# Kernel tuning notes

Hardware: AMD Instinct MI355X
Metric: run time of the kernel (lower is better)

Reference implementation:

```python
import jax, jax.numpy as jnp
import numpy as np

N, H, HEADS = 4096, 256, 3
ALPHA = 0.2
NEG_INF = -9e15


def _sign_adj(key, n, density):
    # sparse signed adjacency with +1 on the diagonal (values in {-1,0,1})
    k1, k2 = jax.random.split(key)
    mask = jax.random.uniform(k1, (n, n)) < density
    sign = jnp.where(jax.random.uniform(k2, (n, n)) < 0.5, -1.0, 1.0)
    adj = jnp.where(mask, sign, 0.0).astype(jnp.float32)
    idx = jnp.arange(n)
    return adj.at[idx, idx].set(1.0)


def setup_inputs() -> dict:
    key = jax.random.key(0)
    ks = jax.random.split(key, 16)
    std = 0.01
    gain = 1.414
    return {
        "h": jax.random.normal(ks[0], (N, H), jnp.float32),
        "node_adj": _sign_adj(ks[1], N, 0.005),
        "edge_adj": _sign_adj(ks[2], N, 0.005),
        "gat_W": jax.random.normal(ks[3], (HEADS, H, H), jnp.float32) * (gain / np.sqrt(H, dtype=np.float32)),
        "gat_a": jax.random.normal(ks[4], (HEADS, 2 * H, 1), jnp.float32) * 0.1,
        "edge_Wih": jax.random.normal(ks[5], (3 * H, H), jnp.float32) * std,
        "edge_Whh": jax.random.normal(ks[6], (3 * H, H), jnp.float32) * std,
        "edge_bih": jnp.zeros((3 * H,), jnp.float32),
        "edge_bhh": jnp.zeros((3 * H,), jnp.float32),
        "node_Wih": jax.random.normal(ks[7], (3 * H, H), jnp.float32) * std,
        "node_Whh": jax.random.normal(ks[8], (3 * H, H), jnp.float32) * std,
        "node_bih": jnp.zeros((3 * H,), jnp.float32),
        "node_bhh": jnp.zeros((3 * H,), jnp.float32),
    }


def _gru_cell(x, hstate, Wih, Whh, bih, bhh):
    # torch.nn.GRUCell math, gate order [r, z, n]
    gi = x @ Wih.T + bih
    gh = hstate @ Whh.T + bhh
    ir, iz, inn = jnp.split(gi, 3, axis=1)
    hr, hz, hn = jnp.split(gh, 3, axis=1)
    r = jax.nn.sigmoid(ir + hr)
    z = jax.nn.sigmoid(iz + hz)
    n = jnp.tanh(inn + r * hn)
    return (1.0 - z) * n + z * hstate


def _gat_head(h, node_adj, edge_adj, W, a):
    hW = h @ W  # [N,H]
    hp = (node_adj > 0).astype(hW.dtype) @ hW
    hm = (node_adj < 0).astype(hW.dtype) @ hW
    e_plus = jax.nn.leaky_relu(jnp.concatenate([hp, hm], axis=1) @ a, ALPHA)[:, 0]   # [N]
    e_minus = jax.nn.leaky_relu(jnp.concatenate([hm, hp], axis=1) @ a, ALPHA)[:, 0]  # [N]
    # attention[i, j] depends only on column j (original builds this via repeat)
    att = jnp.where(edge_adj > 0, e_plus[None, :], NEG_INF)
    att = jnp.where(edge_adj < 0, e_minus[None, :], att)
    att = jax.nn.softmax(att, axis=1)
    return (att * edge_adj) @ hW  # concat=False -> no elu


def reference(h, node_adj, edge_adj, gat_W, gat_a,
              edge_Wih, edge_Whh, edge_bih, edge_bhh,
              node_Wih, node_Whh, node_bih, node_bhh):
    dn = jnp.diag(node_adj)  # [N]
    de = jnp.diag(edge_adj)  # [N]
    idx = jnp.arange(node_adj.shape[0])
    node_adj_norm = node_adj.at[idx, idx].add(-dn)  # zero diagonal
    edge_adj_norm = edge_adj.at[idx, idx].add(-de)

    # msg_type == 'diff'
    node_support = node_adj_norm @ h
    edge_output = _gru_cell(node_support, h, edge_Wih, edge_Whh, edge_bih, edge_bhh)

    edge_support = _gat_head(h, node_adj_norm, edge_adj_norm, gat_W[0], gat_a[0])
    for i in range(1, HEADS):
        edge_support = edge_support + _gat_head(h, node_adj_norm, edge_adj_norm, gat_W[i], gat_a[i])
    edge_support = edge_support / HEADS

    node_output = _gru_cell(edge_support, h, node_Wih, node_Whh, node_bih, node_bhh)

    # sp.mm(I_edge, edge_output) + sp.mm(I_node, node_output)
    return de[:, None] * edge_output + dn[:, None] * node_output
```

## Files before the change

kernel.cpp:

```cpp
#include <hip/hip_runtime.h>
#include <hip/hip_bf16.h>
#include <math.h>

#define NN 4096
#define HH 256
#define G3 768
#define NHEADS 3
#define MAXE 128
#define ALPHA 0.2f

typedef __bf16 bf16;
typedef __attribute__((ext_vector_type(2))) __bf16 bf16x2;
typedef __attribute__((ext_vector_type(4))) __bf16 bf16x4;
typedef __attribute__((ext_vector_type(8))) __bf16 bf16x8;
typedef __attribute__((ext_vector_type(4))) float f32x4;

__device__ __forceinline__ void async_copy16(void* lds, const void* g) {
    __builtin_amdgcn_global_load_lds((const __attribute__((address_space(1))) void*)g,
                                     (__attribute__((address_space(3))) void*)lds, 16, 0, 0);
}

__device__ inline float lrelu(float x) { return x > 0.f ? x : ALPHA * x; }
__device__ inline float sigm(float x) { return 1.f / (1.f + __expf(-x)); }

__global__ __launch_bounds__(256) void prep_k(
    const float* __restrict__ h,
    const float* __restrict__ eWih, const float* __restrict__ eWhh,
    const float* __restrict__ nWih, const float* __restrict__ nWhh,
    const float* __restrict__ gat_W, const float* __restrict__ gat_a,
    bf16* __restrict__ hb,
    bf16* __restrict__ Weib, bf16* __restrict__ Wehb,
    bf16* __restrict__ Wnib, bf16* __restrict__ Wnhb,
    bf16* __restrict__ Wtb, float* __restrict__ c0, float* __restrict__ c1) {
    __shared__ float tile[32][33];
    __shared__ float a_s[512];
    int b = blockIdx.x, t = threadIdx.x;
    if (b < 1024) {
        int idx = b * 256 + t;
        float4 v = *(const float4*)(h + (size_t)idx * 4);
        bf16x4 o = {(bf16)v.x, (bf16)v.y, (bf16)v.z, (bf16)v.w};
        *(bf16x4*)(hb + (size_t)idx * 4) = o;
    } else if (b < 1792) {
        int w = (b - 1024) / 192;
        int idx = ((b - 1024) % 192) * 256 + t;
        const float* in = w == 0 ? eWih : (w == 1 ? eWhh : (w == 2 ? nWih : nWhh));
        bf16* outp = w == 0 ? Weib : (w == 1 ? Wehb : (w == 2 ? Wnib : Wnhb));
        float4 v = *(const float4*)(in + (size_t)idx * 4);
        bf16x4 o = {(bf16)v.x, (bf16)v.y, (bf16)v.z, (bf16)v.w};
        *(bf16x4*)(outp + (size_t)idx * 4) = o;
    } else if (b < 1984) {
        int b2 = b - 1792;
        int hd = b2 >> 6, tl = b2 & 63;
        int k0 = (tl >> 3) * 32, n0 = (tl & 7) * 32;
        int tx = t % 32, ty = t / 32;
        const float* Wh = gat_W + (size_t)hd * HH * HH;
        for (int r = ty; r < 32; r += 8) tile[r][tx] = Wh[(size_t)(k0 + r) * HH + n0 + tx];
        __syncthreads();
        bf16* Wth = Wtb + (size_t)hd * HH * HH;
        for (int r = ty; r < 32; r += 8) Wth[(size_t)(n0 + r) * HH + k0 + tx] = (bf16)tile[tx][r];
    } else {
        int hd = b - 1984;
        a_s[t] = gat_a[(size_t)hd * 512 + t];
        a_s[t + 256] = gat_a[(size_t)hd * 512 + 256 + t];
        __syncthreads();
        const float* Wr = gat_W + (size_t)hd * HH * HH + (size_t)t * HH;
        float s0 = 0.f, s1 = 0.f;
        for (int c = 0; c < HH; c++) {
            float w = Wr[c];
            s0 += w * a_s[c];
            s1 += w * a_s[256 + c];
        }
        c0[hd * HH + t] = s0;
        c1[hd * HH + t] = s1;
    }
}

__global__ __launch_bounds__(256) void scan_k(
    const float* __restrict__ node_adj, const float* __restrict__ edge_adj,
    const bf16* __restrict__ hb,
    const float* __restrict__ c0, const float* __restrict__ c1,
    bf16* __restrict__ nsupb, float* __restrict__ dn, float* __restrict__ de,
    float* __restrict__ ep, float* __restrict__ em,
    int* __restrict__ csr_cols, int* __restrict__ csr_nnz) {
    int i = blockIdx.x, t = threadIdx.x;
    int lane = t & 63, wid = t >> 6;
    __shared__ int cnt;
    __shared__ int cols[256];
    __shared__ float part[6][4];
    if (t == 0) cnt = 0;
    __syncthreads();
    bool node = (blockIdx.y == 0);
    const float* row = (node ? node_adj : edge_adj) + (size_t)i * NN;

    float4 v0 = *(const float4*)(row + t * 4);
    float4 v1 = *(const float4*)(row + t * 4 + 1024);
    float4 v2 = *(const float4*)(row + t * 4 + 2048);
    float4 v3 = *(const float4*)(row + t * 4 + 3072);

#define PELEM(A, J) { float a_ = (A); if (a_ != 0.0f) { \
        if ((J) == i) { (node ? dn : de)[i] = a_; } \
        else { int s_ = atomicAdd(&cnt, 1); if (s_ < 256) cols[s_] = (a_ > 0.0f) ? ((J) + 1) : -((J) + 1); } } }
#define PROC(V, OFS) { if ((V).x != 0.f || (V).y != 0.f || (V).z != 0.f || (V).w != 0.f) { \
        int jb_ = t * 4 + (OFS); \
        PELEM((V).x, jb_) PELEM((V).y, jb_ + 1) PELEM((V).z, jb_ + 2) PELEM((V).w, jb_ + 3) } }
    PROC(v0, 0)
    PROC(v1, 1024)
    PROC(v2, 2048)
    PROC(v3, 3072)
#undef PROC
#undef PELEM

    __syncthreads();
    if (node) {
        int n = cnt < 256 ? cnt : 256;
        float accp = 0.f, accm = 0.f;
#pragma unroll 4
        for (int k = 0; k < n; k++) {
            int c = cols[k];
            int j = (c > 0 ? c : -c) - 1;
            float hv = (float)hb[(size_t)j * HH + t];
            if (c > 0) accp += hv; else accm += hv;
        }
        nsupb[(size_t)i * HH + t] = (bf16)(accp - accm);
        float u[6];
#pragma unroll
        for (int hd = 0; hd < NHEADS; hd++) {
            float a0 = c0[hd * HH + t], a1 = c1[hd * HH + t];
            u[hd * 2]     = accp * a0 + accm * a1;
            u[hd * 2 + 1] = accm * a0 + accp * a1;
        }
#pragma unroll
        for (int vv = 0; vv < 6; vv++)
#pragma unroll
            for (int off = 32; off; off >>= 1) u[vv] += __shfl_xor(u[vv], off);
        if (lane == 0)
#pragma unroll
            for (int vv = 0; vv < 6; vv++) part[vv][wid] = u[vv];
        __syncthreads();
        if (t < 6) {
            float s = part[t][0] + part[t][1] + part[t][2] + part[t][3];
            int hd = t >> 1;
            ((t & 1) == 0 ? ep : em)[(size_t)hd * NN + i] = lrelu(s);
        }
    } else {
        int n = cnt < MAXE ? cnt : MAXE;
        if (t == 0) csr_nnz[i] = n;
        for (int k = t; k < n; k += 256) csr_cols[(size_t)i * MAXE + k] = cols[k];
    }
}

__global__ __launch_bounds__(256) void gemm_bt(
    const bf16* __restrict__ A0, const bf16* __restrict__ A1, const bf16* __restrict__ A2,
    const bf16* __restrict__ B0, const bf16* __restrict__ B1, const bf16* __restrict__ B2,
    bf16* __restrict__ C0, bf16* __restrict__ C1, bf16* __restrict__ C2) {
    __shared__ bf16 a_s[128 * 32];
    __shared__ bf16 b_s[128 * 32];
    int z = blockIdx.z;
    const bf16* A = z == 0 ? A0 : (z == 1 ? A1 : A2);
    const bf16* Bt = z == 0 ? B0 : (z == 1 ? B1 : B2);
    bf16* C = z == 0 ? C0 : (z == 1 ? C1 : C2);

    int tid = threadIdx.x;
    int lane = tid & 63, wid = tid >> 6;
    int wr = (wid >> 1) * 64, wc = (wid & 1) * 64;
    int i0 = blockIdx.x * 128;
    int c0n = blockIdx.y * 128;

    f32x4 acc[4][4] = {};
    int kq = (lane >> 4) * 8;

    for (int k0 = 0; k0 < 256; k0 += 32) {
        __syncthreads();
#pragma unroll
        for (int it = 0; it < 2; it++) {
            int ch = it * 256 + tid;
            int r = ch >> 2, c16 = ch & 3;
            async_copy16(&a_s[ch * 8], A + (size_t)(i0 + r) * 256 + k0 + c16 * 8);
            async_copy16(&b_s[ch * 8], Bt + (size_t)(c0n + r) * 256 + k0 + c16 * 8);
        }
        __syncthreads();
        bf16x8 af[4], bf[4];
#pragma unroll
        for (int m = 0; m < 4; m++) af[m] = *(const bf16x8*)&a_s[(wr + m * 16 + (lane & 15)) * 32 + kq];
#pragma unroll
        for (int n = 0; n < 4; n++) bf[n] = *(const bf16x8*)&b_s[(wc + n * 16 + (lane & 15)) * 32 + kq];
#pragma unroll
        for (int m = 0; m < 4; m++)
#pragma unroll
            for (int n = 0; n < 4; n++)
                acc[m][n] = __builtin_amdgcn_mfma_f32_16x16x32_bf16(af[m], bf[n], acc[m][n], 0, 0, 0);
    }
#pragma unroll
    for (int m = 0; m < 4; m++) {
#pragma unroll
        for (int n = 0; n < 4; n++) {
            int row = i0 + wr + m * 16 + (lane >> 4) * 4;
            int col = c0n + wc + n * 16 + (lane & 15);
#pragma unroll
            for (int j = 0; j < 4; j++)
                C[(size_t)(row + j) * G3 + col] = (bf16)acc[m][n][j];
        }
    }
}

__global__ __launch_bounds__(256) void gat_out(
    const int* __restrict__ csr_cols, const int* __restrict__ csr_nnz,
    const float* __restrict__ ep, const float* __restrict__ em,
    const bf16* __restrict__ hWb2, bf16* __restrict__ esupb) {
    int i = blockIdx.x, t = threadIdx.x;
    __shared__ int cols_s[MAXE];
    __shared__ int js[MAXE];
    __shared__ float w_s[NHEADS][MAXE];
    int n = csr_nnz[i];
    if (t < MAXE && t < n) {
        int c = csr_cols[(size_t)i * MAXE + t];
        cols_s[t] = c;
        js[t] = (c > 0 ? c : -c) - 1;
    }
    __syncthreads();
    int wid = t >> 6, lane = t & 63;
    if (wid < NHEADS) {
        int hd = wid;
        const float* eph = ep + (size_t)hd * NN;
        const float* emh = em + (size_t)hd * NN;
        float v0 = -1e30f, v1 = -1e30f;
        if (lane < n)      { int c = cols_s[lane];      v0 = c > 0 ? eph[js[lane]]      : emh[js[lane]]; }
        if (lane + 64 < n) { int c = cols_s[lane + 64]; v1 = c > 0 ? eph[js[lane + 64]] : emh[js[lane + 64]]; }
        float mx = fmaxf(v0, v1);
#pragma unroll
        for (int off = 32; off; off >>= 1) mx = fmaxf(mx, __shfl_xor(mx, off));
        float w0 = (lane < n) ? __expf(v0 - mx) : 0.f;
        float w1 = (lane + 64 < n) ? __expf(v1 - mx) : 0.f;
        float s = w0 + w1;
#pragma unroll
        for (int off = 32; off; off >>= 1) s += __shfl_xor(s, off);
        float inv = 1.f / s;
        if (lane < n)      w_s[hd][lane]      = (cols_s[lane] > 0 ? w0 : -w0) * inv;
        if (lane + 64 < n) w_s[hd][lane + 64] = (cols_s[lane + 64] > 0 ? w1 : -w1) * inv;
    }
    __syncthreads();
    float acc = 0.f;
#pragma unroll
    for (int hd = 0; hd < NHEADS; hd++) {
        const bf16* base = hWb2 + (size_t)hd * HH + t;
#pragma unroll 4
        for (int k = 0; k < n; k++)
            acc += w_s[hd][k] * (float)base[(size_t)js[k] * G3];
    }
    esupb[(size_t)i * HH + t] = (bf16)(acc * (1.f / 3.f));
}

__global__ __launch_bounds__(256) void gru_both(
    const bf16* __restrict__ gie, const bf16* __restrict__ ghe,
    const bf16* __restrict__ gin, const bf16* __restrict__ ghn,
    const float* __restrict__ ebih, const float* __restrict__ ebhh,
    const float* __restrict__ nbih, const float* __restrict__ nbhh,
    const float* __restrict__ h, const float* __restrict__ dnv, const float* __restrict__ dev,
    float* __restrict__ out) {
    int sub = threadIdx.x >> 7, tc = threadIdx.x & 127;
    int i = blockIdx.x * 2 + sub;
    int c = tc * 2;
    size_t gb = (size_t)i * G3;
    float2 hv = *(const float2*)(h + (size_t)i * HH + c);
    float De = dev[i], Dn = dnv[i];

#define LD2(p, off) (*(const bf16x2*)((p) + gb + (off) + c))
#define BI2(p, off) (*(const float2*)((p) + (off) + c))
    bf16x2 eir = LD2(gie, 0), eiz = LD2(gie, 256), ein = LD2(gie, 512);
    bf16x2 ehr = LD2(ghe, 0), ehz = LD2(ghe, 256), ehn = LD2(ghe, 512);
    bf16x2 nir = LD2(gin, 0), niz = LD2(gin, 256), nin = LD2(gin, 512);
    bf16x2 nhr = LD2(ghn, 0), nhz = LD2(ghn, 256), nhn = LD2(ghn, 512);
    float2 ebr = BI2(ebih, 0), ebz = BI2(ebih, 256), ebn = BI2(ebih, 512);
    float2 eb2r = BI2(ebhh, 0), eb2z = BI2(ebhh, 256), eb2n = BI2(ebhh, 512);
    float2 nbr = BI2(nbih, 0), nbz = BI2(nbih, 256), nbn = BI2(nbih, 512);
    float2 nb2r = BI2(nbhh, 0), nb2z = BI2(nbhh, 256), nb2n = BI2(nbhh, 512);
#undef LD2
#undef BI2

    float res[2];
#pragma unroll
    for (int j = 0; j < 2; j++) {
        float hj = j == 0 ? hv.x : hv.y;
        float r = sigm(((float)eir[j] + (j ? ebr.y : ebr.x)) + ((float)ehr[j] + (j ? eb2r.y : eb2r.x)));
        float z = sigm(((float)eiz[j] + (j ? ebz.y : ebz.x)) + ((float)ehz[j] + (j ? eb2z.y : eb2z.x)));
        float nv = tanhf(((float)ein[j] + (j ? ebn.y : ebn.x)) + r * ((float)ehn[j] + (j ? eb2n.y : eb2n.x)));
        float eo = (1.f - z) * nv + z * hj;
        float r2 = sigm(((float)nir[j] + (j ? nbr.y : nbr.x)) + ((float)nhr[j] + (j ? nb2r.y : nb2r.x)));
        float z2 = sigm(((float)niz[j] + (j ? nbz.y : nbz.x)) + ((float)nhz[j] + (j ? nb2z.y : nb2z.x)));
        float nv2 = tanhf(((float)nin[j] + (j ? nbn.y : nbn.x)) + r2 * ((float)nhn[j] + (j ? nb2n.y : nb2n.x)));
        float no = (1.f - z2) * nv2 + z2 * hj;
        res[j] = De * eo + Dn * no;
    }
    *(float2*)(out + (size_t)i * HH + c) = make_float2(res[0], res[1]);
}

extern "C" void kernel_launch(void* const* d_in, const int* in_sizes, int n_in,
                              void* d_out, int out_size, void* d_ws, size_t ws_size,
                              hipStream_t stream) {
    const float* h        = (const float*)d_in[0];
    const float* node_adj = (const float*)d_in[1];
    const float* edge_adj = (const float*)d_in[2];
    const float* gat_W    = (const float*)d_in[3];
    const float* gat_a    = (const float*)d_in[4];
    const float* e_Wih    = (const float*)d_in[5];
    const float* e_Whh    = (const float*)d_in[6];
    const float* e_bih    = (const float*)d_in[7];
    const float* e_bhh    = (const float*)d_in[8];
    const float* n_Wih    = (const float*)d_in[9];
    const float* n_Whh    = (const float*)d_in[10];
    const float* n_bih    = (const float*)d_in[11];
    const float* n_bhh    = (const float*)d_in[12];
    float* out = (float*)d_out;

    char* ws = (char*)d_ws;
    size_t off = 0;
    auto alloc = [&](size_t bytes) { char* p = ws + off; off += (bytes + 255) & ~(size_t)255; return p; };

    float* ep    = (float*)alloc((size_t)NHEADS * NN * 4);
    float* em    = (float*)alloc((size_t)NHEADS * NN * 4);
    float* c0    = (float*)alloc((size_t)NHEADS * HH * 4);
    float* c1    = (float*)alloc((size_t)NHEADS * HH * 4);
    float* dn    = (float*)alloc(NN * 4);
    float* de    = (float*)alloc(NN * 4);
    bf16*  hb    = (bf16*)alloc((size_t)NN * HH * 2);
    bf16*  nsupb = (bf16*)alloc((size_t)NN * HH * 2);
    bf16*  esupb = (bf16*)alloc((size_t)NN * HH * 2);
    bf16*  hWb2  = (bf16*)alloc((size_t)NN * G3 * 2);
    bf16*  gie   = (bf16*)alloc((size_t)NN * G3 * 2);
    bf16*  ghe   = (bf16*)alloc((size_t)NN * G3 * 2);
    bf16*  gin   = (bf16*)alloc((size_t)NN * G3 * 2);
    bf16*  ghn   = (bf16*)alloc((size_t)NN * G3 * 2);
    bf16*  Weib  = (bf16*)alloc((size_t)G3 * HH * 2);
    bf16*  Wehb  = (bf16*)alloc((size_t)G3 * HH * 2);
    bf16*  Wnib  = (bf16*)alloc((size_t)G3 * HH * 2);
    bf16*  Wnhb  = (bf16*)alloc((size_t)G3 * HH * 2);
    bf16*  Wtb   = (bf16*)alloc((size_t)NHEADS * HH * HH * 2);
    int*   csr_cols = (int*)alloc((size_t)NN * MAXE * 4);
    int*   csr_nnz  = (int*)alloc(NN * 4);

    dim3 b256(256);

    prep_k<<<1987, b256, 0, stream>>>(h, e_Wih, e_Whh, n_Wih, n_Whh, gat_W, gat_a,
                                      hb, Weib, Wehb, Wnib, Wnhb, Wtb, c0, c1);

    scan_k<<<dim3(NN, 2), b256, 0, stream>>>(node_adj, edge_adj, hb, c0, c1,
                                             nsupb, dn, de, ep, em, csr_cols, csr_nnz);

    gemm_bt<<<dim3(NN / 128, G3 / 128, 3), b256, 0, stream>>>(
        hb, nsupb, hb, Wtb, Weib, Wehb, hWb2, gie, ghe);

    gat_out<<<NN, b256, 0, stream>>>(csr_cols, csr_nnz, ep, em, hWb2, esupb);

    gemm_bt<<<dim3(NN / 128, G3 / 128, 2), b256, 0, stream>>>(
        esupb, hb, hb, Wnib, Wnhb, Wnhb, gin, ghn, ghn);

    gru_both<<<NN / 2, b256, 0, stream>>>(gie, ghe, gin, ghn,
                                          e_bih, e_bhh, n_bih, n_bhh,
                                          h, dn, de, out);
}
```

Measured before the change: 95.99 us.

## Map one wavefront per adjacency row in scan and vectorize gather loops

```diff
diff --git a/kernel.cpp b/kernel.cpp
--- a/kernel.cpp
+++ b/kernel.cpp
@@ -64,14 +64,17 @@
         a_s[t + 256] = gat_a[(size_t)hd * 512 + 256 + t];
         __syncthreads();
         const float* Wr = gat_W + (size_t)hd * HH * HH + (size_t)t * HH;
-        float s0 = 0.f, s1 = 0.f;
-        for (int c = 0; c < HH; c++) {
-            float w = Wr[c];
-            s0 += w * a_s[c];
-            s1 += w * a_s[256 + c];
-        }
-        c0[hd * HH + t] = s0;
-        c1[hd * HH + t] = s1;
+        f32x4 s0v = {}, s1v = {};
+#pragma unroll 8
+        for (int c4 = 0; c4 < 64; c4++) {
+            f32x4 w = *(const f32x4*)(Wr + c4 * 4);
+            f32x4 a0 = *(const f32x4*)(a_s + c4 * 4);
+            f32x4 a1 = *(const f32x4*)(a_s + 256 + c4 * 4);
+            s0v += w * a0;
+            s1v += w * a1;
+        }
+        c0[hd * HH + t] = s0v[0] + s0v[1] + s0v[2] + s0v[3];
+        c1[hd * HH + t] = s1v[0] + s1v[1] + s1v[2] + s1v[3];
     }
 }
 
@@ -82,70 +85,89 @@
     bf16* __restrict__ nsupb, float* __restrict__ dn, float* __restrict__ de,
     float* __restrict__ ep, float* __restrict__ em,
     int* __restrict__ csr_cols, int* __restrict__ csr_nnz) {
-    int i = blockIdx.x, t = threadIdx.x;
-    int lane = t & 63, wid = t >> 6;
-    __shared__ int cnt;
-    __shared__ int cols[256];
-    __shared__ float part[6][4];
-    if (t == 0) cnt = 0;
-    __syncthreads();
+    int t = threadIdx.x, lane = t & 63, wid = t >> 6;
+    int i = blockIdx.x * 4 + wid;
     bool node = (blockIdx.y == 0);
-    const float* row = (node ? node_adj : edge_adj) + (size_t)i * NN;
-
-    float4 v0 = *(const float4*)(row + t * 4);
-    float4 v1 = *(const float4*)(row + t * 4 + 1024);
-    float4 v2 = *(const float4*)(row + t * 4 + 2048);
-    float4 v3 = *(const float4*)(row + t * 4 + 3072);
-
-#define PELEM(A, J) { float a_ = (A); if (a_ != 0.0f) { \
-        if ((J) == i) { (node ? dn : de)[i] = a_; } \
-        else { int s_ = atomicAdd(&cnt, 1); if (s_ < 256) cols[s_] = (a_ > 0.0f) ? ((J) + 1) : -((J) + 1); } } }
-#define PROC(V, OFS) { if ((V).x != 0.f || (V).y != 0.f || (V).z != 0.f || (V).w != 0.f) { \
-        int jb_ = t * 4 + (OFS); \
-        PELEM((V).x, jb_) PELEM((V).y, jb_ + 1) PELEM((V).z, jb_ + 2) PELEM((V).w, jb_ + 3) } }
-    PROC(v0, 0)
-    PROC(v1, 1024)
-    PROC(v2, 2048)
-    PROC(v3, 3072)
-#undef PROC
-#undef PELEM
-
-    __syncthreads();
+    __shared__ int cnt[4];
+    __shared__ int cols[4][MAXE];
+    if (lane == 0) cnt[wid] = 0;
+    __syncthreads();
+
+    float* dia = node ? dn : de;
+    const float* rp = (node ? node_adj : edge_adj) + (size_t)i * NN + lane * 4;
+
+    f32x4 v0  = *(const f32x4*)(rp);
+    f32x4 v1  = *(const f32x4*)(rp + 256);
+    f32x4 v2  = *(const f32x4*)(rp + 512);
+    f32x4 v3  = *(const f32x4*)(rp + 768);
+    f32x4 v4  = *(const f32x4*)(rp + 1024);
+    f32x4 v5  = *(const f32x4*)(rp + 1280);
+    f32x4 v6  = *(const f32x4*)(rp + 1536);
+    f32x4 v7  = *(const f32x4*)(rp + 1792);
+    f32x4 v8  = *(const f32x4*)(rp + 2048);
+    f32x4 v9  = *(const f32x4*)(rp + 2304);
+    f32x4 v10 = *(const f32x4*)(rp + 2560);
+    f32x4 v11 = *(const f32x4*)(rp + 2816);
+    f32x4 v12 = *(const f32x4*)(rp + 3072);
+    f32x4 v13 = *(const f32x4*)(rp + 3328);
+    f32x4 v14 = *(const f32x4*)(rp + 3584);
+    f32x4 v15 = *(const f32x4*)(rp + 3840);
+
+#define PEL(A, J) { float a_ = (A); if (a_ != 0.0f) { \
+        if ((J) == i) { dia[i] = a_; } \
+        else { int s_ = atomicAdd(&cnt[wid], 1); if (s_ < MAXE) cols[wid][s_] = (a_ > 0.0f) ? ((J) + 1) : -((J) + 1); } } }
+#define PV(V, Q) { if ((V)[0] != 0.f || (V)[1] != 0.f || (V)[2] != 0.f || (V)[3] != 0.f) { \
+        int jb_ = (Q) * 256 + lane * 4; \
+        PEL((V)[0], jb_) PEL((V)[1], jb_ + 1) PEL((V)[2], jb_ + 2) PEL((V)[3], jb_ + 3) } }
+    PV(v0, 0)  PV(v1, 1)  PV(v2, 2)  PV(v3, 3)
+    PV(v4, 4)  PV(v5, 5)  PV(v6, 6)  PV(v7, 7)
+    PV(v8, 8)  PV(v9, 9)  PV(v10, 10) PV(v11, 11)
+    PV(v12, 12) PV(v13, 13) PV(v14, 14) PV(v15, 15)
+#undef PV
+#undef PEL
+
+    __syncthreads();
+    int n = cnt[wid];
+    if (n > MAXE) n = MAXE;
+
     if (node) {
-        int n = cnt < 256 ? cnt : 256;
-        float accp = 0.f, accm = 0.f;
+        f32x4 accp = {}, accm = {};
 #pragma unroll 4
         for (int k = 0; k < n; k++) {
-            int c = cols[k];
+            int c = cols[wid][k];
             int j = (c > 0 ? c : -c) - 1;
-            float hv = (float)hb[(size_t)j * HH + t];
-            if (c > 0) accp += hv; else accm += hv;
-        }
-        nsupb[(size_t)i * HH + t] = (bf16)(accp - accm);
+            bf16x4 hv = *(const bf16x4*)(hb + (size_t)j * HH + lane * 4);
+            f32x4 f = {(float)hv[0], (float)hv[1], (float)hv[2], (float)hv[3]};
+            if (c > 0) accp += f; else accm += f;
+        }
+        f32x4 d = accp - accm;
+        bf16x4 o = {(bf16)d[0], (bf16)d[1], (bf16)d[2], (bf16)d[3]};
+        *(bf16x4*)(nsupb + (size_t)i * HH + lane * 4) = o;
+
         float u[6];
 #pragma unroll
         for (int hd = 0; hd < NHEADS; hd++) {
-            float a0 = c0[hd * HH + t], a1 = c1[hd * HH + t];
-            u[hd * 2]     = accp * a0 + accm * a1;
-            u[hd * 2 + 1] = accm * a0 + accp * a1;
+            f32x4 a0 = *(const f32x4*)(c0 + hd * HH + lane * 4);
+            f32x4 a1 = *(const f32x4*)(c1 + hd * HH + lane * 4);
+            f32x4 up = accp * a0 + accm * a1;
+            f32x4 um = accm * a0 + accp * a1;
+            u[hd * 2]     = up[0] + up[1] + up[2] + up[3];
+            u[hd * 2 + 1] = um[0] + um[1] + um[2] + um[3];
         }
 #pragma unroll
         for (int vv = 0; vv < 6; vv++)
 #pragma unroll
             for (int off = 32; off; off >>= 1) u[vv] += __shfl_xor(u[vv], off);
-        if (lane == 0)
-#pragma unroll
-            for (int vv = 0; vv < 6; vv++) part[vv][wid] = u[vv];
-        __syncthreads();
-        if (t < 6) {
-            float s = part[t][0] + part[t][1] + part[t][2] + part[t][3];
-            int hd = t >> 1;
-            ((t & 1) == 0 ? ep : em)[(size_t)hd * NN + i] = lrelu(s);
+        if (lane == 0) {
+#pragma unroll
+            for (int hd = 0; hd < NHEADS; hd++) {
+                ep[(size_t)hd * NN + i] = lrelu(u[hd * 2]);
+                em[(size_t)hd * NN + i] = lrelu(u[hd * 2 + 1]);
+            }
         }
     } else {
-        int n = cnt < MAXE ? cnt : MAXE;
-        if (t == 0) csr_nnz[i] = n;
-        for (int k = t; k < n; k += 256) csr_cols[(size_t)i * MAXE + k] = cols[k];
+        if (lane == 0) csr_nnz[i] = n;
+        for (int k = lane; k < n; k += 64) csr_cols[(size_t)i * MAXE + k] = cols[wid][k];
     }
 }
 
@@ -211,8 +233,9 @@
     __shared__ int cols_s[MAXE];
     __shared__ int js[MAXE];
     __shared__ float w_s[NHEADS][MAXE];
+    __shared__ f32x4 sacc[NHEADS][64];
     int n = csr_nnz[i];
-    if (t < MAXE && t < n) {
+    if (t < n) {
         int c = csr_cols[(size_t)i * MAXE + t];
         cols_s[t] = c;
         js[t] = (c > 0 ? c : -c) - 1;
@@ -239,15 +262,25 @@
         if (lane + 64 < n) w_s[hd][lane + 64] = (cols_s[lane + 64] > 0 ? w1 : -w1) * inv;
     }
     __syncthreads();
-    float acc = 0.f;
-#pragma unroll
-    for (int hd = 0; hd < NHEADS; hd++) {
-        const bf16* base = hWb2 + (size_t)hd * HH + t;
+    if (t < 192) {
+        int hd = t >> 6, g = t & 63;
+        const bf16* base = hWb2 + (size_t)hd * HH + g * 4;
+        f32x4 acc = {};
 #pragma unroll 4
-        for (int k = 0; k < n; k++)
-            acc += w_s[hd][k] * (float)base[(size_t)js[k] * G3];
-    }
-    esupb[(size_t)i * HH + t] = (bf16)(acc * (1.f / 3.f));
+        for (int k = 0; k < n; k++) {
+            float w = w_s[hd][k];
+            bf16x4 hv = *(const bf16x4*)(base + (size_t)js[k] * G3);
+            f32x4 f = {(float)hv[0], (float)hv[1], (float)hv[2], (float)hv[3]};
+            acc += w * f;
+        }
+        sacc[hd][g] = acc;
+    }
+    __syncthreads();
+    if (t < 64) {
+        f32x4 s = (sacc[0][t] + sacc[1][t] + sacc[2][t]) * (1.f / 3.f);
+        bf16x4 o = {(bf16)s[0], (bf16)s[1], (bf16)s[2], (bf16)s[3]};
+        *(bf16x4*)(esupb + (size_t)i * HH + t * 4) = o;
+    }
 }
 
 __global__ __launch_bounds__(256) void gru_both(
@@ -343,8 +376,8 @@
     prep_k<<<1987, b256, 0, stream>>>(h, e_Wih, e_Whh, n_Wih, n_Whh, gat_W, gat_a,
                                       hb, Weib, Wehb, Wnib, Wnhb, Wtb, c0, c1);
 
-    scan_k<<<dim3(NN, 2), b256, 0, stream>>>(node_adj, edge_adj, hb, c0, c1,
-                                             nsupb, dn, de, ep, em, csr_cols, csr_nnz);
+    scan_k<<<dim3(NN / 4, 2), b256, 0, stream>>>(node_adj, edge_adj, hb, c0, c1,
+                                                 nsupb, dn, de, ep, em, csr_cols, csr_nnz);
 
     gemm_bt<<<dim3(NN / 128, G3 / 128, 3), b256, 0, stream>>>(
         hb, nsupb, hb, Wtb, Weib, Wehb, hWb2, gie, ghe);
```

Result: faster. 85.96 us (-10.4%).
